# Performance work log

Hardware: AMD Instinct MI355X
Metric: run time of the kernel (lower is better)

Reference implementation:

```python
import jax, jax.numpy as jnp
import numpy as np

B, L, E, H = 2, 2048, 1024, 16
D = E // H


def _complex_linear(xr, xi, Wr, Wi, br, bi):
    # (xr + i*xi) @ (Wr + i*Wi)^T + (br + i*bi)
    yr = xr @ Wr.T - xi @ Wi.T + br
    yi = xr @ Wi.T + xi @ Wr.T + bi
    return yr, yi


def _split_heads(x):
    # [B, L, E] -> [B, H, L, D]
    return x.reshape(B, -1, H, D).transpose(0, 2, 1, 3)


def setup_inputs() -> dict:
    key = jax.random.key(0)
    ks = jax.random.split(key, 32)
    s = 1.0 / np.sqrt(E)
    inp = {}
    names = ["query_r", "query_i", "key_r", "key_i", "value_r", "value_i"]
    for i, n in enumerate(names):
        inp[n] = jax.random.normal(ks[i], (B, L, E), dtype=jnp.float32)
    j = 6
    for p in ["q", "k", "v", "o"]:
        inp[f"W{p}_r"] = jax.random.normal(ks[j], (E, E), dtype=jnp.float32) * s; j += 1
        inp[f"W{p}_i"] = jax.random.normal(ks[j], (E, E), dtype=jnp.float32) * s; j += 1
        inp[f"b{p}_r"] = jax.random.normal(ks[j], (E,), dtype=jnp.float32) * 0.01; j += 1
        inp[f"b{p}_i"] = jax.random.normal(ks[j], (E,), dtype=jnp.float32) * 0.01; j += 1
    return inp


def reference(query_r, query_i, key_r, key_i, value_r, value_i,
              Wq_r, Wq_i, bq_r, bq_i,
              Wk_r, Wk_i, bk_r, bk_i,
              Wv_r, Wv_i, bv_r, bv_i,
              Wo_r, Wo_i, bo_r, bo_i):
    qr, qi = _complex_linear(query_r, query_i, Wq_r, Wq_i, bq_r, bq_i)
    kr, ki = _complex_linear(key_r, key_i, Wk_r, Wk_i, bk_r, bk_i)
    vr, vi = _complex_linear(value_r, value_i, Wv_r, Wv_i, bv_r, bv_i)
    qr, qi = _split_heads(qr), _split_heads(qi)
    kr, ki = _split_heads(kr), _split_heads(ki)
    vr, vi = _split_heads(vr), _split_heads(vi)
    scale = jnp.float32(1.0 / np.sqrt(D))
    # Re(q @ conj(k)^T) = qr.kr^T + qi.ki^T  (imag part of scores is discarded)
    scores = (jnp.einsum('bhld,bhmd->bhlm', qr, kr)
              + jnp.einsum('bhld,bhmd->bhlm', qi, ki)) * scale
    probs = jax.nn.softmax(scores, axis=-1)  # real probs
    out_r = jnp.einsum('bhlm,bhmd->bhld', probs, vr)
    out_i = jnp.einsum('bhlm,bhmd->bhld', probs, vi)
    out_r = out_r.transpose(0, 2, 1, 3).reshape(B, L, E)
    out_i = out_i.transpose(0, 2, 1, 3).reshape(B, L, E)
    yr, yi = _complex_linear(out_r, out_i, Wo_r, Wo_i, bo_r, bo_i)
    return jnp.stack([yr, yi])  # [2, B, L, E] = (real, imag)
```

## Files before the change

### kernel.cpp

```cpp
#include <hip/hip_runtime.h>


#define LL 2048
#define EE 1024
#define HH 16
#define BL 4096
#define KK 2048

typedef __attribute__((ext_vector_type(8))) short bf16x8;
typedef __attribute__((ext_vector_type(4))) float f32x4;
typedef unsigned short u16;

__device__ __forceinline__ u16 f2bf(float x) {
    unsigned u = __builtin_bit_cast(unsigned, x);
    u += 0x7fff + ((u >> 16) & 1);
    return (u16)(u >> 16);
}

__device__ __forceinline__ void gl2lds16(const void* g, void* l) {
    __builtin_amdgcn_global_load_lds((const __attribute__((address_space(1))) void*)g,
                                     (__attribute__((address_space(3))) void*)l, 16, 0, 0);
}

struct ConvXArgs { const float* src[6]; u16* dst[6]; };
__global__ void conv_x(ConvXArgs a) {
    const int z = blockIdx.y;
    int i = blockIdx.x * 256 + threadIdx.x;
    float4 v = ((const float4*)a.src[z])[i];
    ushort4 o;
    o.x = f2bf(v.x); o.y = f2bf(v.y); o.z = f2bf(v.z); o.w = f2bf(v.w);
    ((ushort4*)a.dst[z])[i] = o;
}

struct ConvWArgs { const float* wr[4]; const float* wi[4]; u16* w2[4]; };
__global__ void conv_w(ConvWArgs a) {
    const int z = blockIdx.y;
    int i = blockIdx.x * 256 + threadIdx.x;
    int n = i >> 9, k = (i & 511) << 2;
    bool nh = n >= EE, kh = k >= EE;
    int nn = n & (EE - 1), kk = k & (EE - 1);
    const float* src = nh ? (kh ? a.wr[z] : a.wi[z]) : (kh ? a.wi[z] : a.wr[z]);
    float sgn = (!nh && kh) ? -1.0f : 1.0f;
    float4 v = *(const float4*)(src + nn * EE + kk);
    ushort4 o;
    o.x = f2bf(v.x * sgn); o.y = f2bf(v.y * sgn);
    o.z = f2bf(v.z * sgn); o.w = f2bf(v.w * sgn);
    *(ushort4*)(a.w2[z] + n * KK + k) = o;
}

#define GEMM_BK64_LOOP(Ar, Ai, B2)                                             \
    for (int k0 = 0; k0 < KK; k0 += 64) {                                      \
        const u16* Asrc = (k0 < EE) ? (Ar + k0) : (Ai + (k0 - EE));            \
        const u16* Bsrc = B2 + k0;                                             \
        __syncthreads();                                                       \
        {                                                                      \
            int rr = lane >> 3, cg = (lane & 7) ^ rr;                          \
            for (int t = 0; t < 4; t++) {                                      \
                int s = wave * 4 + t;                                          \
                int r0 = s * 8 + rr;                                           \
                gl2lds16(Asrc + (size_t)(m0 + r0) * EE + cg * 8, &As[s * 512]);\
                gl2lds16(Bsrc + (size_t)(n0 + r0) * KK + cg * 8, &Bs[s * 512]);\
            }                                                                  \
        }                                                                      \
        __syncthreads();                                                       \
        for (int ks2 = 0; ks2 < 2; ks2++) {                                    \
            bf16x8 a[4], b[4];                                                 \
            for (int t = 0; t < 4; t++) {                                      \
                int ra = wm + t * 16 + l16;                                    \
                a[t] = *(const bf16x8*)&As[ra * 64 + (((ks2 * 4 + quad) ^ (ra & 7)) << 3)]; \
                int rb = wn + t * 16 + l16;                                    \
                b[t] = *(const bf16x8*)&Bs[rb * 64 + (((ks2 * 4 + quad) ^ (rb & 7)) << 3)]; \
            }                                                                  \
            for (int i = 0; i < 4; i++)                                        \
                for (int j = 0; j < 4; j++)                                    \
                    acc[i][j] = __builtin_amdgcn_mfma_f32_16x16x32_bf16(a[i], b[j], acc[i][j], 0, 0, 0); \
        }                                                                      \
    }

struct QKVArgs {
    const u16* Ar[3]; const u16* Ai[3]; const u16* B2[3];
    const float* br[3]; const float* bi[3];
    u16* out[3];
    float oscale[3];
};

__launch_bounds__(256, 3)
__global__ void gemm_qkv(QKVArgs args) {
    __shared__ __attribute__((aligned(16))) u16 As[128 * 64];
    __shared__ __attribute__((aligned(16))) u16 Bs[128 * 64];

    const int z = blockIdx.z;
    const u16* __restrict__ Ar = args.Ar[z];
    const u16* __restrict__ Ai = args.Ai[z];
    const u16* __restrict__ B2 = args.B2[z];

    const int tid = threadIdx.x, wave = tid >> 6, lane = tid & 63;
    const int quad = lane >> 4, l16 = lane & 15;
    const int m0 = blockIdx.y * 128, n0 = blockIdx.x * 128;
    const int wm = (wave >> 1) * 64, wn = (wave & 1) * 64;

    f32x4 acc[4][4] = {};

    GEMM_BK64_LOOP(Ar, Ai, B2)

    const float* __restrict__ br_ = args.br[z];
    const float* __restrict__ bi_ = args.bi[z];
    u16* __restrict__ out = args.out[z];
    const float oscale = args.oscale[z];

    for (int j = 0; j < 4; j++) {
        int gn = n0 + wn + j * 16 + l16;
        int ri = gn >> 10, e = gn & 1023;
        float bias = ri ? bi_[e] : br_[e];
        for (int i = 0; i < 4; i++) {
            int gmb = m0 + wm + i * 16 + quad * 4;
            for (int r = 0; r < 4; r++) {
                int gm = gmb + r;
                float v = (acc[i][j][r] + bias) * oscale;
                int b = gm >> 11, l = gm & 2047;
                int h = e >> 6, d = e & 63;
                if (z < 2)
                    out[((b * HH + h) * LL + l) * 128 + ri * 64 + d] = f2bf(v);
                else
                    out[((b * HH + h) * 128 + ri * 64 + d) * LL + l] = f2bf(v);
            }
        }
    }
}

__launch_bounds__(256, 2)
__global__ void gemm_oproj(const u16* __restrict__ Ar, const u16* __restrict__ Ai,
                           const u16* __restrict__ B2,
                           const float* __restrict__ br, const float* __restrict__ bi,
                           float* __restrict__ out)
{
    __shared__ __attribute__((aligned(16))) u16 As[128 * 64];
    __shared__ __attribute__((aligned(16))) u16 Bs[128 * 64];

    const int tid = threadIdx.x, wave = tid >> 6, lane = tid & 63;
    const int quad = lane >> 4, l16 = lane & 15;
    const int m0 = blockIdx.y * 128, n0 = blockIdx.x * 128;
    const int wm = (wave >> 1) * 64, wn = (wave & 1) * 64;

    f32x4 acc[4][4] = {};

    GEMM_BK64_LOOP(Ar, Ai, B2)

    for (int j = 0; j < 4; j++) {
        int gn = n0 + wn + j * 16 + l16;
        int ri = gn >> 10, e = gn & 1023;
        float bias = ri ? bi[e] : br[e];
        for (int i = 0; i < 4; i++) {
            int gmb = m0 + wm + i * 16 + quad * 4;
            for (int r = 0; r < 4; r++) {
                int gm = gmb + r;
                out[ri * (BL * EE) + gm * EE + e] = acc[i][j][r] + bias;
            }
        }
    }
}

__launch_bounds__(256, 3)
__global__ void attn(const u16* __restrict__ q_ws, const u16* __restrict__ k_ws,
                     const u16* __restrict__ v_ws,
                     u16* __restrict__ o_r, u16* __restrict__ o_i)
{
    __shared__ __attribute__((aligned(16))) u16 kbuf[2][64 * 128];
    __shared__ __attribute__((aligned(16))) u16 vbuf[128 * 64];
    __shared__ __attribute__((aligned(16))) float red_sh[4][16];

    const int tid = threadIdx.x, wave = tid >> 6, lane = tid & 63;
    const int quad = lane >> 4, l16 = lane & 15;
    const int q0 = blockIdx.x * 64, bh = blockIdx.y;

    bf16x8 qf[4];
    {
        const u16* qp = q_ws + (size_t)(bh * LL + q0 + wave * 16 + l16) * 128 + quad * 8;
        for (int ks = 0; ks < 4; ks++)
            qf[ks] = *(const bf16x8*)(qp + ks * 32);
    }

    auto stage_k = [&](int nb, int kv0) {
        for (int t = 0; t < 4; t++) {
            int s = wave * 4 + t;
            int row = s * 4 + (lane >> 4);
            int cg = (lane & 15) ^ (row & 15);
            gl2lds16(k_ws + (size_t)(bh * LL + kv0 + row) * 128 + cg * 8, &kbuf[nb][s * 512]);
        }
    };
    auto stage_v = [&](int kv0) {
        for (int t = 0; t < 4; t++) {
            int s = wave * 4 + t;
            int row = s * 8 + (lane >> 3);
            int cg = (lane & 7) ^ (row & 7);
            gl2lds16(v_ws + (size_t)(bh * 128 + row) * LL + kv0 + cg * 8, &vbuf[s * 512]);
        }
    };

    stage_k(0, 0);
    stage_v(0);
    stage_k(1, 64);
    __syncthreads();

    f32x4 oacc[8] = {};
    float m_st = -__builtin_inff();
    float l_st = 0.f;

    for (int N = 0; N < 32; N++) {
        const int cur = N & 1;
        u16* K = kbuf[cur];

        f32x4 s[4] = {};
        for (int ks = 0; ks < 4; ks++) {
            bf16x8 kf[4];
            for (int mt = 0; mt < 4; mt++) {
                int row = mt * 16 + l16;
                int cl = (ks * 4 + quad) ^ (row & 15);
                kf[mt] = *(const bf16x8*)&K[row * 128 + cl * 8];
            }
            for (int mt = 0; mt < 4; mt++)
                s[mt] = __builtin_amdgcn_mfma_f32_16x16x32_bf16(kf[mt], qf[ks], s[mt], 0, 0, 0);
        }

        bool changed = false;
        float alpha;
        {
            float mx = -__builtin_inff();
            for (int mt = 0; mt < 4; mt++)
                for (int r = 0; r < 4; r++)
                    mx = fmaxf(mx, s[mt][r]);
            mx = fmaxf(mx, __shfl_xor(mx, 16, 64));
            mx = fmaxf(mx, __shfl_xor(mx, 32, 64));
            float mnew = fmaxf(m_st, mx);
            changed = (mnew != m_st);
            alpha = __builtin_amdgcn_exp2f(m_st - mnew);
            m_st = mnew;
            float sum = 0.f;
            for (int mt = 0; mt < 4; mt++)
                for (int r = 0; r < 4; r++) {
                    float p = __builtin_amdgcn_exp2f(s[mt][r] - mnew);
                    s[mt][r] = p;
                    sum += p;
                }
            sum += __shfl_xor(sum, 16, 64);
            sum += __shfl_xor(sum, 32, 64);
            l_st = l_st * alpha + sum;
            if (quad == 0) red_sh[wave][l16] = alpha;
        }
        __syncthreads();

        u16* P = kbuf[cur] + wave * 1024;
        for (int mt = 0; mt < 4; mt++) {
            int q = l16;
            int cg = mt * 2 + (quad >> 1);
            int cl = cg ^ (q & 7);
            ushort4 pk;
            pk.x = f2bf(s[mt][0]); pk.y = f2bf(s[mt][1]);
            pk.z = f2bf(s[mt][2]); pk.w = f2bf(s[mt][3]);
            *(ushort4*)&P[q * 64 + cl * 8 + (quad & 1) * 4] = pk;
        }

        if (__any(changed)) {
            f32x4 av = *(const f32x4*)&red_sh[wave][quad * 4];
            for (int nt = 0; nt < 8; nt++)
                oacc[nt] *= av;
        }

        for (int ks = 0; ks < 2; ks++) {
            int clp = (ks * 4 + quad) ^ (l16 & 7);
            bf16x8 pf = *(const bf16x8*)&P[l16 * 64 + clp * 8];
            for (int nt = 0; nt < 8; nt++) {
                int row = nt * 16 + l16;
                int cl = (ks * 4 + quad) ^ (row & 7);
                bf16x8 vf = *(const bf16x8*)&vbuf[row * 64 + cl * 8];
                oacc[nt] = __builtin_amdgcn_mfma_f32_16x16x32_bf16(pf, vf, oacc[nt], 0, 0, 0);
            }
        }
        __syncthreads();

        if (N + 2 < 32) stage_k(cur, (N + 2) * 64);
        if (N + 1 < 32) stage_v((N + 1) * 64);
    }

    if (quad == 0) red_sh[wave][l16] = l_st;
    __syncthreads();
    f32x4 lv = *(const f32x4*)&red_sh[wave][quad * 4];
    f32x4 inv;
    for (int r = 0; r < 4; r++) inv[r] = 1.0f / lv[r];
    const int b = bh >> 4, h = bh & 15;
    for (int nt = 0; nt < 8; nt++) {
        int d2 = nt * 16 + l16;
        u16* op = (d2 < 64) ? o_r : o_i;
        int col = h * 64 + (d2 & 63);
        for (int r = 0; r < 4; r++) {
            int l = q0 + wave * 16 + quad * 4 + r;
            op[(size_t)(b * LL + l) * EE + col] = f2bf(oacc[nt][r] * inv[r]);
        }
    }
}

extern "C" void kernel_launch(void* const* d_in, const int* in_sizes, int n_in,
                              void* d_out, int out_size, void* d_ws, size_t ws_size,
                              hipStream_t stream) {
    const float* bq_r = (const float*)d_in[8];
    const float* bq_i = (const float*)d_in[9];
    const float* bk_r = (const float*)d_in[12];
    const float* bk_i = (const float*)d_in[13];
    const float* bv_r = (const float*)d_in[16];
    const float* bv_i = (const float*)d_in[17];
    const float* bo_r = (const float*)d_in[20];
    const float* bo_i = (const float*)d_in[21];

    u16* ws = (u16*)d_ws;
    const size_t XN = 4194304;
    u16* xqr = ws;            u16* xqi = xqr + XN;
    u16* xkr = xqi + XN;      u16* xki = xkr + XN;
    u16* xvr = xki + XN;      u16* xvi = xvr + XN;
    u16* w2q = xvi + XN;
    u16* w2k = w2q + XN;
    u16* w2v = w2k + XN;
    u16* w2o = w2v + XN;
    u16* q_ws = w2o + XN;
    u16* k_ws = q_ws + 8388608;
    u16* v_ws = k_ws + 8388608;
    u16* o_r = xqr;
    u16* o_i = xqr + XN;

    dim3 blk(256);

    ConvXArgs cx;
    cx.src[0] = (const float*)d_in[0]; cx.dst[0] = xqr;
    cx.src[1] = (const float*)d_in[1]; cx.dst[1] = xqi;
    cx.src[2] = (const float*)d_in[2]; cx.dst[2] = xkr;
    cx.src[3] = (const float*)d_in[3]; cx.dst[3] = xki;
    cx.src[4] = (const float*)d_in[4]; cx.dst[4] = xvr;
    cx.src[5] = (const float*)d_in[5]; cx.dst[5] = xvi;
    conv_x<<<dim3(4096, 6), blk, 0, stream>>>(cx);

    ConvWArgs cw;
    cw.wr[0] = (const float*)d_in[6];  cw.wi[0] = (const float*)d_in[7];  cw.w2[0] = w2q;
    cw.wr[1] = (const float*)d_in[10]; cw.wi[1] = (const float*)d_in[11]; cw.w2[1] = w2k;
    cw.wr[2] = (const float*)d_in[14]; cw.wi[2] = (const float*)d_in[15]; cw.w2[2] = w2v;
    cw.wr[3] = (const float*)d_in[18]; cw.wi[3] = (const float*)d_in[19]; cw.w2[3] = w2o;
    conv_w<<<dim3(4096, 4), blk, 0, stream>>>(cw);

    const float QSCALE = 0.125f * 1.44269504088896f;
    QKVArgs qa;
    qa.Ar[0] = xqr; qa.Ai[0] = xqi; qa.B2[0] = w2q; qa.br[0] = bq_r; qa.bi[0] = bq_i; qa.out[0] = q_ws; qa.oscale[0] = QSCALE;
    qa.Ar[1] = xkr; qa.Ai[1] = xki; qa.B2[1] = w2k; qa.br[1] = bk_r; qa.bi[1] = bk_i; qa.out[1] = k_ws; qa.oscale[1] = 1.0f;
    qa.Ar[2] = xvr; qa.Ai[2] = xvi; qa.B2[2] = w2v; qa.br[2] = bv_r; qa.bi[2] = bv_i; qa.out[2] = v_ws; qa.oscale[2] = 1.0f;
    gemm_qkv<<<dim3(16, 32, 3), blk, 0, stream>>>(qa);

    attn<<<dim3(32, 32), blk, 0, stream>>>(q_ws, k_ws, v_ws, o_r, o_i);

    gemm_oproj<<<dim3(16, 32), blk, 0, stream>>>(o_r, o_i, w2o, bo_r, bo_i, (float*)d_out);
}
```

Measured before the change: 486.4 us.

## Rewrite QKV GEMM as 256x256 tile, 8-wave, double-buffered pipelined kernel

```diff
diff --git a/kernel.cpp b/kernel.cpp
--- a/kernel.cpp
+++ b/kernel.cpp
@@ -84,45 +84,136 @@
     float oscale[3];
 };
 
-__launch_bounds__(256, 3)
+#define BAR      asm volatile("s_barrier" ::: "memory")
+#define BARW(N)  asm volatile("s_waitcnt vmcnt(" #N ")\n\ts_barrier" ::: "memory")
+
+#define LOAD_A(QM)                                                             \
+    { const u16* base_ = &AB[buf][0][QM][0];                                   \
+      _Pragma("unroll") for (int i_ = 0; i_ < 4; i_++) {                       \
+          int row_ = wr * 64 + i_ * 16 + l16;                                  \
+          _Pragma("unroll") for (int s_ = 0; s_ < 2; s_++) {                   \
+              int ph_ = (s_ * 4 + quad) ^ (l16 & 7);                           \
+              afr[i_][s_] = *(const bf16x8*)&base_[row_ * 64 + ph_ * 8];       \
+          } } }
+
+#define LOAD_B(QN)                                                             \
+    { const u16* base_ = &AB[buf][1][QN][0];                                   \
+      _Pragma("unroll") for (int j_ = 0; j_ < 2; j_++) {                       \
+          int row_ = wc * 32 + j_ * 16 + l16;                                  \
+          _Pragma("unroll") for (int s_ = 0; s_ < 2; s_++) {                   \
+              int ph_ = (s_ * 4 + quad) ^ (l16 & 7);                           \
+              bfr[QN][j_][s_] = *(const bf16x8*)&base_[row_ * 64 + ph_ * 8];   \
+          } } }
+
+#define MMA(QM, QN)                                                            \
+    { __builtin_amdgcn_s_setprio(1);                                           \
+      _Pragma("unroll") for (int s_ = 0; s_ < 2; s_++)                         \
+          _Pragma("unroll") for (int i_ = 0; i_ < 4; i_++)                     \
+              _Pragma("unroll") for (int j_ = 0; j_ < 2; j_++)                 \
+                  acc[QM * 4 + i_][QN * 2 + j_] =                              \
+                      __builtin_amdgcn_mfma_f32_16x16x32_bf16(                 \
+                          afr[i_][s_], bfr[QN][j_][s_],                        \
+                          acc[QM * 4 + i_][QN * 2 + j_], 0, 0, 0);             \
+      __builtin_amdgcn_s_setprio(0); }
+
+#define STAGE_A(BUF, HALF, K0)                                                 \
+    { const u16* S_ = ((K0) < EE) ? (Apr + (K0)) : (Api + ((K0) - EE));        \
+      int rl_ = wv * 8 + (lane >> 3);                                          \
+      int cg_ = ((lane & 7) ^ (lane >> 3)) * 8;                                \
+      gl2lds16(S_ + (size_t)(m0 + (HALF) * 128 + rl_) * EE + cg_,              \
+               &AB[BUF][0][HALF][wv * 512]);                                   \
+      gl2lds16(S_ + (size_t)(m0 + (HALF) * 128 + rl_ + 64) * EE + cg_,         \
+               &AB[BUF][0][HALF][wv * 512 + 4096]); }
+
+#define STAGE_B(BUF, HALF, K0)                                                 \
+    { const u16* S_ = Bp + (K0);                                               \
+      int rl_ = wv * 8 + (lane >> 3);                                          \
+      int cg_ = ((lane & 7) ^ (lane >> 3)) * 8;                                \
+      gl2lds16(S_ + (size_t)(n0 + (HALF) * 128 + rl_) * (size_t)KK + cg_,      \
+               &AB[BUF][1][HALF][wv * 512]);                                   \
+      gl2lds16(S_ + (size_t)(n0 + (HALF) * 128 + rl_ + 64) * (size_t)KK + cg_, \
+               &AB[BUF][1][HALF][wv * 512 + 4096]); }
+
+__launch_bounds__(512, 2)
 __global__ void gemm_qkv(QKVArgs args) {
-    __shared__ __attribute__((aligned(16))) u16 As[128 * 64];
-    __shared__ __attribute__((aligned(16))) u16 Bs[128 * 64];
+    __shared__ __attribute__((aligned(16))) u16 AB[2][2][2][8192];
 
     const int z = blockIdx.z;
-    const u16* __restrict__ Ar = args.Ar[z];
-    const u16* __restrict__ Ai = args.Ai[z];
-    const u16* __restrict__ B2 = args.B2[z];
-
-    const int tid = threadIdx.x, wave = tid >> 6, lane = tid & 63;
+    const u16* __restrict__ Apr = args.Ar[z];
+    const u16* __restrict__ Api = args.Ai[z];
+    const u16* __restrict__ Bp  = args.B2[z];
+
+    const int tid = threadIdx.x, wv = tid >> 6, lane = tid & 63;
     const int quad = lane >> 4, l16 = lane & 15;
-    const int m0 = blockIdx.y * 128, n0 = blockIdx.x * 128;
-    const int wm = (wave >> 1) * 64, wn = (wave & 1) * 64;
-
-    f32x4 acc[4][4] = {};
-
-    GEMM_BK64_LOOP(Ar, Ai, B2)
+    const int m0 = blockIdx.y * 256, n0 = blockIdx.x * 256;
+    const int wr = wv >> 2, wc = wv & 3;
+
+    f32x4 acc[8][4] = {};
+    bf16x8 afr[4][2];
+    bf16x8 bfr[2][2][2];
+
+    STAGE_A(0, 0, 0); STAGE_B(0, 0, 0); STAGE_B(0, 1, 0); STAGE_A(0, 1, 0);
+    BARW(4);
+
+    for (int T = 0; T < 31; T++) {
+        const int buf = T & 1, nb = buf ^ 1;
+        const int k1 = T * 64 + 64;
+        LOAD_A(0); LOAD_B(0);
+        STAGE_A(nb, 0, k1);
+        BAR;
+        MMA(0, 0);
+        BARW(4);
+        LOAD_B(1);
+        STAGE_B(nb, 0, k1);
+        BAR;
+        MMA(0, 1);
+        BARW(4);
+        LOAD_A(1);
+        STAGE_B(nb, 1, k1);
+        BAR;
+        MMA(1, 1);
+        BAR;
+        STAGE_A(nb, 1, k1);
+        BAR;
+        MMA(1, 0);
+        BARW(4);
+    }
+    {
+        const int buf = 1;
+        LOAD_A(0); LOAD_B(0);
+        MMA(0, 0);
+        BARW(2);
+        LOAD_B(1);
+        MMA(0, 1);
+        BARW(0);
+        LOAD_A(1);
+        MMA(1, 1);
+        MMA(1, 0);
+    }
 
     const float* __restrict__ br_ = args.br[z];
     const float* __restrict__ bi_ = args.bi[z];
     u16* __restrict__ out = args.out[z];
     const float oscale = args.oscale[z];
 
+    #pragma unroll
     for (int j = 0; j < 4; j++) {
-        int gn = n0 + wn + j * 16 + l16;
+        int gn = n0 + (j >> 1) * 128 + wc * 32 + (j & 1) * 16 + l16;
         int ri = gn >> 10, e = gn & 1023;
         float bias = ri ? bi_[e] : br_[e];
-        for (int i = 0; i < 4; i++) {
-            int gmb = m0 + wm + i * 16 + quad * 4;
+        int h = e >> 6, d = e & 63;
+        #pragma unroll
+        for (int i = 0; i < 8; i++) {
+            int gmb = m0 + (i >> 2) * 128 + wr * 64 + (i & 3) * 16 + quad * 4;
+            #pragma unroll
             for (int r = 0; r < 4; r++) {
                 int gm = gmb + r;
                 float v = (acc[i][j][r] + bias) * oscale;
                 int b = gm >> 11, l = gm & 2047;
-                int h = e >> 6, d = e & 63;
                 if (z < 2)
-                    out[((b * HH + h) * LL + l) * 128 + ri * 64 + d] = f2bf(v);
+                    out[((size_t)(b * HH + h) * LL + l) * 128 + ri * 64 + d] = f2bf(v);
                 else
-                    out[((b * HH + h) * 128 + ri * 64 + d) * LL + l] = f2bf(v);
+                    out[((size_t)(b * HH + h) * 128 + ri * 64 + d) * LL + l] = f2bf(v);
             }
         }
     }
@@ -349,7 +440,7 @@
     qa.Ar[0] = xqr; qa.Ai[0] = xqi; qa.B2[0] = w2q; qa.br[0] = bq_r; qa.bi[0] = bq_i; qa.out[0] = q_ws; qa.oscale[0] = QSCALE;
     qa.Ar[1] = xkr; qa.Ai[1] = xki; qa.B2[1] = w2k; qa.br[1] = bk_r; qa.bi[1] = bk_i; qa.out[1] = k_ws; qa.oscale[1] = 1.0f;
     qa.Ar[2] = xvr; qa.Ai[2] = xvi; qa.B2[2] = w2v; qa.br[2] = bv_r; qa.bi[2] = bv_i; qa.out[2] = v_ws; qa.oscale[2] = 1.0f;
-    gemm_qkv<<<dim3(16, 32, 3), blk, 0, stream>>>(qa);
+    gemm_qkv<<<dim3(8, 16, 3), dim3(512), 0, stream>>>(qa);
 
     attn<<<dim3(32, 32), blk, 0, stream>>>(q_ws, k_ws, v_ws, o_r, o_i);
 
```

Measured after the change: 492.9 us. Within noise of the previous version (+1.3%).

## Triple-buffer LDS GEMM pipeline with 512-thread 128x256 tiles

Applied to the files above, without the earlier changes.

```diff
diff --git a/kernel.cpp b/kernel.cpp
--- a/kernel.cpp
+++ b/kernel.cpp
@@ -48,34 +48,73 @@
     *(ushort4*)(a.w2[z] + n * KK + k) = o;
 }
 
-#define GEMM_BK64_LOOP(Ar, Ai, B2)                                             \
-    for (int k0 = 0; k0 < KK; k0 += 64) {                                      \
-        const u16* Asrc = (k0 < EE) ? (Ar + k0) : (Ai + (k0 - EE));            \
-        const u16* Bsrc = B2 + k0;                                             \
-        __syncthreads();                                                       \
-        {                                                                      \
-            int rr = lane >> 3, cg = (lane & 7) ^ rr;                          \
-            for (int t = 0; t < 4; t++) {                                      \
-                int s = wave * 4 + t;                                          \
-                int r0 = s * 8 + rr;                                           \
-                gl2lds16(Asrc + (size_t)(m0 + r0) * EE + cg * 8, &As[s * 512]);\
-                gl2lds16(Bsrc + (size_t)(n0 + r0) * KK + cg * 8, &Bs[s * 512]);\
-            }                                                                  \
-        }                                                                      \
-        __syncthreads();                                                       \
-        for (int ks2 = 0; ks2 < 2; ks2++) {                                    \
-            bf16x8 a[4], b[4];                                                 \
-            for (int t = 0; t < 4; t++) {                                      \
-                int ra = wm + t * 16 + l16;                                    \
-                a[t] = *(const bf16x8*)&As[ra * 64 + (((ks2 * 4 + quad) ^ (ra & 7)) << 3)]; \
-                int rb = wn + t * 16 + l16;                                    \
-                b[t] = *(const bf16x8*)&Bs[rb * 64 + (((ks2 * 4 + quad) ^ (rb & 7)) << 3)]; \
-            }                                                                  \
-            for (int i = 0; i < 4; i++)                                        \
-                for (int j = 0; j < 4; j++)                                    \
-                    acc[i][j] = __builtin_amdgcn_mfma_f32_16x16x32_bf16(a[i], b[j], acc[i][j], 0, 0, 0); \
-        }                                                                      \
-    }
+#define BAR      asm volatile("s_barrier" ::: "memory")
+#define BARW(N)  asm volatile("s_waitcnt vmcnt(" #N ")\n\ts_barrier" ::: "memory")
+
+#define S_A(B, K0)                                                             \
+    { const u16* S_ = ((K0) < EE) ? (Apr + (K0)) : (Api + ((K0) - EE));        \
+      int rl_ = wv * 8 + (lane >> 3);                                          \
+      int cg_ = ((lane & 7) ^ (lane >> 3)) * 8;                                \
+      gl2lds16(S_ + (size_t)(m0 + rl_) * EE + cg_, &As3[B][wv * 512]);         \
+      gl2lds16(S_ + (size_t)(m0 + rl_ + 64) * EE + cg_, &As3[B][wv * 512 + 4096]); }
+
+#define S_B(B, H, K0)                                                          \
+    { const u16* S_ = Bp + (K0);                                               \
+      int rl_ = wv * 8 + (lane >> 3);                                          \
+      int cg_ = ((lane & 7) ^ (lane >> 3)) * 8;                                \
+      gl2lds16(S_ + (size_t)(n0 + (H) * 128 + rl_) * (size_t)KK + cg_,         \
+               &Bs3[B][(H) * 8192 + wv * 512]);                                \
+      gl2lds16(S_ + (size_t)(n0 + (H) * 128 + rl_ + 64) * (size_t)KK + cg_,    \
+               &Bs3[B][(H) * 8192 + wv * 512 + 4096]); }
+
+#define L_A(B)                                                                 \
+    _Pragma("unroll") for (int i_ = 0; i_ < 4; i_++) {                         \
+        int row_ = wr * 64 + i_ * 16 + l16;                                    \
+        _Pragma("unroll") for (int s_ = 0; s_ < 2; s_++) {                     \
+            int ph_ = (s_ * 4 + quad) ^ (l16 & 7);                             \
+            afr[i_][s_] = *(const bf16x8*)&As3[B][row_ * 64 + ph_ * 8]; } }
+
+#define L_B(B, H)                                                              \
+    _Pragma("unroll") for (int j_ = 0; j_ < 2; j_++) {                         \
+        int row_ = wc * 32 + j_ * 16 + l16;                                    \
+        _Pragma("unroll") for (int s_ = 0; s_ < 2; s_++) {                     \
+            int ph_ = (s_ * 4 + quad) ^ (l16 & 7);                             \
+            bfr[j_][s_] = *(const bf16x8*)&Bs3[B][(H) * 8192 + row_ * 64 + ph_ * 8]; } }
+
+#define MMA_H(H)                                                               \
+    { __builtin_amdgcn_s_setprio(1);                                           \
+      _Pragma("unroll") for (int s_ = 0; s_ < 2; s_++)                         \
+          _Pragma("unroll") for (int i_ = 0; i_ < 4; i_++)                     \
+              _Pragma("unroll") for (int j_ = 0; j_ < 2; j_++)                 \
+                  acc[i_][(H) * 2 + j_] =                                      \
+                      __builtin_amdgcn_mfma_f32_16x16x32_bf16(                 \
+                          afr[i_][s_], bfr[j_][s_], acc[i_][(H) * 2 + j_], 0, 0, 0); \
+      __builtin_amdgcn_s_setprio(0); }
+
+#define GITER(B, NB, KN)                                                       \
+    {   L_A(B); L_B(B, 0);                                                     \
+        S_A(NB, KN); S_B(NB, 0, KN);                                           \
+        BAR;                                                                   \
+        MMA_H(0);                                                              \
+        L_B(B, 1);                                                             \
+        S_B(NB, 1, KN);                                                        \
+        BAR;                                                                   \
+        MMA_H(1);                                                              \
+        BARW(6); }
+
+#define GEMM3_LOOP                                                             \
+    S_A(0, 0);  S_B(0, 0, 0);  S_B(0, 1, 0);                                   \
+    S_A(1, 64); S_B(1, 0, 64); S_B(1, 1, 64);                                  \
+    BARW(6);                                                                   \
+    for (int t3 = 0; t3 < 10; t3++) {                                          \
+        const int kb = t3 * 192;                                               \
+        GITER(0, 2, kb + 128);                                                 \
+        GITER(1, 0, kb + 192);                                                 \
+        GITER(2, 1, kb + 256);                                                 \
+    }                                                                          \
+    { L_A(0); L_B(0, 0); MMA_H(0); L_B(0, 1); MMA_H(1); }                      \
+    BARW(0);                                                                   \
+    { L_A(1); L_B(1, 0); MMA_H(0); L_B(1, 1); MMA_H(1); }
 
 struct QKVArgs {
     const u16* Ar[3]; const u16* Ai[3]; const u16* B2[3];
@@ -84,74 +123,88 @@
     float oscale[3];
 };
 
-__launch_bounds__(256, 3)
+__launch_bounds__(512, 1)
 __global__ void gemm_qkv(QKVArgs args) {
-    __shared__ __attribute__((aligned(16))) u16 As[128 * 64];
-    __shared__ __attribute__((aligned(16))) u16 Bs[128 * 64];
+    __shared__ __attribute__((aligned(16))) u16 As3[3][128 * 64];
+    __shared__ __attribute__((aligned(16))) u16 Bs3[3][256 * 64];
 
     const int z = blockIdx.z;
-    const u16* __restrict__ Ar = args.Ar[z];
-    const u16* __restrict__ Ai = args.Ai[z];
-    const u16* __restrict__ B2 = args.B2[z];
-
-    const int tid = threadIdx.x, wave = tid >> 6, lane = tid & 63;
+    const u16* __restrict__ Apr = args.Ar[z];
+    const u16* __restrict__ Api = args.Ai[z];
+    const u16* __restrict__ Bp  = args.B2[z];
+
+    const int tid = threadIdx.x, wv = tid >> 6, lane = tid & 63;
     const int quad = lane >> 4, l16 = lane & 15;
-    const int m0 = blockIdx.y * 128, n0 = blockIdx.x * 128;
-    const int wm = (wave >> 1) * 64, wn = (wave & 1) * 64;
+    const int m0 = blockIdx.y * 128, n0 = blockIdx.x * 256;
+    const int wr = wv >> 2, wc = wv & 3;
 
     f32x4 acc[4][4] = {};
-
-    GEMM_BK64_LOOP(Ar, Ai, B2)
+    bf16x8 afr[4][2];
+    bf16x8 bfr[2][2];
+
+    GEMM3_LOOP
 
     const float* __restrict__ br_ = args.br[z];
     const float* __restrict__ bi_ = args.bi[z];
     u16* __restrict__ out = args.out[z];
     const float oscale = args.oscale[z];
 
+    #pragma unroll
     for (int j = 0; j < 4; j++) {
-        int gn = n0 + wn + j * 16 + l16;
+        int gn = n0 + (j >> 1) * 128 + wc * 32 + (j & 1) * 16 + l16;
         int ri = gn >> 10, e = gn & 1023;
         float bias = ri ? bi_[e] : br_[e];
+        int h = e >> 6, d = e & 63;
+        #pragma unroll
         for (int i = 0; i < 4; i++) {
-            int gmb = m0 + wm + i * 16 + quad * 4;
+            int gmb = m0 + wr * 64 + i * 16 + quad * 4;
+            #pragma unroll
             for (int r = 0; r < 4; r++) {
                 int gm = gmb + r;
                 float v = (acc[i][j][r] + bias) * oscale;
                 int b = gm >> 11, l = gm & 2047;
-                int h = e >> 6, d = e & 63;
                 if (z < 2)
-                    out[((b * HH + h) * LL + l) * 128 + ri * 64 + d] = f2bf(v);
+                    out[((size_t)(b * HH + h) * LL + l) * 128 + ri * 64 + d] = f2bf(v);
                 else
-                    out[((b * HH + h) * 128 + ri * 64 + d) * LL + l] = f2bf(v);
+                    out[((size_t)(b * HH + h) * 128 + ri * 64 + d) * LL + l] = f2bf(v);
             }
         }
     }
 }
 
-__launch_bounds__(256, 2)
+__launch_bounds__(512, 1)
 __global__ void gemm_oproj(const u16* __restrict__ Ar, const u16* __restrict__ Ai,
                            const u16* __restrict__ B2,
                            const float* __restrict__ br, const float* __restrict__ bi,
                            float* __restrict__ out)
 {
-    __shared__ __attribute__((aligned(16))) u16 As[128 * 64];
-    __shared__ __attribute__((aligned(16))) u16 Bs[128 * 64];
-
-    const int tid = threadIdx.x, wave = tid >> 6, lane = tid & 63;
+    __shared__ __attribute__((aligned(16))) u16 As3[3][128 * 64];
+    __shared__ __attribute__((aligned(16))) u16 Bs3[3][256 * 64];
+
+    const u16* __restrict__ Apr = Ar;
+    const u16* __restrict__ Api = Ai;
+    const u16* __restrict__ Bp  = B2;
+
+    const int tid = threadIdx.x, wv = tid >> 6, lane = tid & 63;
     const int quad = lane >> 4, l16 = lane & 15;
-    const int m0 = blockIdx.y * 128, n0 = blockIdx.x * 128;
-    const int wm = (wave >> 1) * 64, wn = (wave & 1) * 64;
+    const int m0 = blockIdx.y * 128, n0 = blockIdx.x * 256;
+    const int wr = wv >> 2, wc = wv & 3;
 
     f32x4 acc[4][4] = {};
-
-    GEMM_BK64_LOOP(Ar, Ai, B2)
-
+    bf16x8 afr[4][2];
+    bf16x8 bfr[2][2];
+
+    GEMM3_LOOP
+
+    #pragma unroll
     for (int j = 0; j < 4; j++) {
-        int gn = n0 + wn + j * 16 + l16;
+        int gn = n0 + (j >> 1) * 128 + wc * 32 + (j & 1) * 16 + l16;
         int ri = gn >> 10, e = gn & 1023;
         float bias = ri ? bi[e] : br[e];
+        #pragma unroll
         for (int i = 0; i < 4; i++) {
-            int gmb = m0 + wm + i * 16 + quad * 4;
+            int gmb = m0 + wr * 64 + i * 16 + quad * 4;
+            #pragma unroll
             for (int r = 0; r < 4; r++) {
                 int gm = gmb + r;
                 out[ri * (BL * EE) + gm * EE + e] = acc[i][j][r] + bias;
@@ -349,9 +402,9 @@
     qa.Ar[0] = xqr; qa.Ai[0] = xqi; qa.B2[0] = w2q; qa.br[0] = bq_r; qa.bi[0] = bq_i; qa.out[0] = q_ws; qa.oscale[0] = QSCALE;
     qa.Ar[1] = xkr; qa.Ai[1] = xki; qa.B2[1] = w2k; qa.br[1] = bk_r; qa.bi[1] = bk_i; qa.out[1] = k_ws; qa.oscale[1] = 1.0f;
     qa.Ar[2] = xvr; qa.Ai[2] = xvi; qa.B2[2] = w2v; qa.br[2] = bv_r; qa.bi[2] = bv_i; qa.out[2] = v_ws; qa.oscale[2] = 1.0f;
-    gemm_qkv<<<dim3(16, 32, 3), blk, 0, stream>>>(qa);
+    gemm_qkv<<<dim3(8, 32, 3), dim3(512), 0, stream>>>(qa);
 
     attn<<<dim3(32, 32), blk, 0, stream>>>(q_ws, k_ws, v_ws, o_r, o_i);
 
-    gemm_oproj<<<dim3(16, 32), blk, 0, stream>>>(o_r, o_i, w2o, bo_r, bo_i, (float*)d_out);
-}
+    gemm_oproj<<<dim3(8, 32), dim3(512), 0, stream>>>(o_r, o_i, w2o, bo_r, bo_i, (float*)d_out);
+}
```

Measured after the change: 477.3 us. About the same (-1.9%).
